# Performance work log

Measured on AMD Instinct MI355X. Metric: run time of the kernel, lower is better.

The kernel has to match this reference:

```python
import math
import jax, jax.numpy as jnp
import numpy as np

# dims: layers, batch, seq, hidden, heads, ffn-mult
L, B, S, D, H, FFN = 2, 4, 2048, 256, 8, 4
HD = D // H          # head dim (= head v dim, double_v_dim=False)
EPS = 1e-5
SCALE_BASE = 512


def _ln(x, w, b):
    mu = x.mean(-1, keepdims=True)
    var = x.var(-1, keepdims=True)
    return (x - mu) * jax.lax.rsqrt(var + EPS) * w + b


def _xpos_tables():
    half = HD // 2
    sv = (np.arange(0, HD, 2) + 0.4 * HD) / (1.4 * HD)            # [half]
    pos = np.arange(S, dtype=np.float64)
    scale = sv[None, :] ** (pos[:, None] / SCALE_BASE)            # [S, half]
    inv_freq = 1.0 / (10000.0 ** (np.arange(half) / half))
    ang = pos[:, None] * inv_freq[None, :]                        # [S, half]
    return (jnp.asarray(np.sin(ang), jnp.float32),
            jnp.asarray(np.cos(ang), jnp.float32),
            jnp.asarray(scale, jnp.float32))

SIN, COS, XSCALE = _xpos_tables()


def _xpos(x, downscale=False):
    # x: [B, H, S, HD]
    sc = 1.0 / XSCALE if downscale else XSCALE
    sin2 = jnp.repeat(SIN * sc, 2, axis=-1)                       # [S, HD]
    cos2 = jnp.repeat(COS * sc, 2, axis=-1)
    x1, x2 = x[..., 0::2], x[..., 1::2]
    xr = jnp.stack((-x2, x1), axis=-1).reshape(x.shape)           # rotate_every_two
    return x * cos2 + xr * sin2


def _decay_mask():
    g = 1.0 - jnp.exp(jnp.linspace(math.log(1 / 32), math.log(1 / 512), H))
    n = jnp.arange(S)[:, None]
    m = jnp.arange(S)[None, :]
    keep = n >= m
    expo = jnp.where(keep, n - m, 0).astype(jnp.float32)
    return jnp.where(keep, g[:, None, None] ** expo[None], 0.0)   # [H, S, S]

DMASK = _decay_mask()


def setup_inputs() -> dict:
    key = jax.random.key(0)
    ks = jax.random.split(key, 16)
    sc = 1.0 / D
    f32 = jnp.float32
    return {
        "X":     jax.random.normal(ks[0], (B, S, D), f32),
        "Wq":    jax.random.normal(ks[1], (L, D, D), f32) * sc,
        "Wk":    jax.random.normal(ks[2], (L, D, D), f32) * sc,
        "Wv":    jax.random.normal(ks[3], (L, D, D), f32) * sc,
        "Wg":    jax.random.normal(ks[4], (L, D, D), f32) * sc,
        "Wo":    jax.random.normal(ks[5], (L, D, D), f32) * sc,
        "gn_w":  jnp.ones((L, D), f32) + 0.02 * jax.random.normal(ks[6], (L, D), f32),
        "gn_b":  0.02 * jax.random.normal(ks[7], (L, D), f32),
        "ln1_w": jnp.ones((L, D), f32),
        "ln1_b": jnp.zeros((L, D), f32),
        "ln2_w": jnp.ones((L, D), f32),
        "ln2_b": jnp.zeros((L, D), f32),
        "w1":    jax.random.normal(ks[8], (L, D, FFN * D), f32) * 0.02,
        "b1":    0.02 * jax.random.normal(ks[9], (L, FFN * D), f32),
        "w2":    jax.random.normal(ks[10], (L, FFN * D, D), f32) * 0.02,
        "b2":    0.02 * jax.random.normal(ks[11], (L, D), f32),
        "lnf_w": jnp.ones((D,), f32),
        "lnf_b": jnp.zeros((D,), f32),
    }


def reference(X, Wq, Wk, Wv, Wg, Wo, gn_w, gn_b, ln1_w, ln1_b,
              ln2_w, ln2_b, w1, b1, w2, b2, lnf_w, lnf_b):
    x = X
    for i in range(L):
        xn = _ln(x, ln1_w[i], ln1_b[i])                           # [B,S,D]
        q = (xn @ Wq[i]).reshape(B, S, H, HD).transpose(0, 2, 1, 3)
        k = (xn @ Wk[i]).reshape(B, S, H, HD).transpose(0, 2, 1, 3)
        v = (xn @ Wv[i]).reshape(B, S, H, HD).transpose(0, 2, 1, 3)
        q = _xpos(q)
        k = _xpos(k, downscale=True)
        att = jnp.einsum('bhnd,bhmd->bhnm', q, k) * DMASK          # [B,H,S,S]
        y = jnp.einsum('bhnm,bhmd->bhnd', att, v)                  # [B,H,S,HD]
        # GroupNorm(heads, v_dim): per-(b, position, head) normalization
        mu = y.mean(-1, keepdims=True)
        var = y.var(-1, keepdims=True)
        y = (y - mu) * jax.lax.rsqrt(var + EPS)
        y = y.transpose(0, 2, 1, 3).reshape(B, S, D)               # concat heads
        y = y * gn_w[i] + gn_b[i]
        g = xn @ Wg[i]
        ret = (g * jax.nn.sigmoid(g) * y) @ Wo[i]                  # swish gate + out proj
        yres = ret + x
        yn = _ln(yres, ln2_w[i], ln2_b[i])
        f = jax.nn.gelu(yn @ w1[i] + b1[i], approximate=False) @ w2[i] + b2[i]
        x = _ln(f + yres, lnf_w, lnf_b)
    return x
```

## Files before the change

kernel.cpp:

```cpp
#include <hip/hip_runtime.h>
#include <hip/hip_bf16.h>

typedef __hip_bfloat16 bf16;
typedef unsigned short ushort_t;
typedef __attribute__((ext_vector_type(8))) short short8v;
typedef __attribute__((ext_vector_type(4))) float f32x4;
typedef __attribute__((ext_vector_type(4))) unsigned int uint4v;

#define LYR 2
#define BB 4
#define SS 2048
#define DD 256
#define HH 8
#define HDD 32
#define FFD 1024
#define MM (BB*SS)

__device__ __forceinline__ unsigned int cvtpk(float lo, float hi) {
  unsigned int r;
  asm("v_cvt_pk_bf16_f32 %0, %1, %2" : "=v"(r) : "v"(lo), "v"(hi));
  return r;
}
__device__ __forceinline__ ushort_t f2b1(float x) { return (ushort_t)cvtpk(x, x); }

__device__ __forceinline__ void gload_lds16(const void* g, void* l) {
  __builtin_amdgcn_global_load_lds((const __attribute__((address_space(1))) void*)g,
                                   (__attribute__((address_space(3))) void*)l, 16, 0, 0);
}

__device__ __forceinline__ float l2g_of(int h) {
  return log2f(1.0f - expf(-3.4657359028f - 0.3960841187f * (float)h));
}

struct WDesc { const float* src; bf16* dst; int K; int N; };
struct WDescA { WDesc d[14]; float* tsn; float* tcs; float* tsc; };
__global__ __launch_bounds__(256) void wconv_k(WDescA da) {
  if (blockIdx.z == 14) {
    int i = (blockIdx.y * 32 + blockIdx.x) * 256 + threadIdx.y * 32 + threadIdx.x;
    if (i >= SS * 16) return;
    int s = i >> 4, j = i & 15;
    float sv = (2.0f * (float)j + 0.4f * (float)HDD) / (1.4f * (float)HDD);
    da.tsc[i] = powf(sv, (float)s * (1.0f / 512.0f));
    float inv_freq = powf(10000.0f, -(float)j * (1.0f / 16.0f));
    float ang = (float)s * inv_freq;
    da.tsn[i] = sinf(ang);
    da.tcs[i] = cosf(ang);
    return;
  }
  WDesc dd = da.d[blockIdx.z];
  int n0 = blockIdx.x * 32, k0 = blockIdx.y * 32;
  if (n0 >= dd.N || k0 >= dd.K) return;
  __shared__ float t[32][33];
  int tx = threadIdx.x, ty = threadIdx.y;
  #pragma unroll
  for (int i = 0; i < 32; i += 8) t[ty + i][tx] = dd.src[(size_t)(k0 + ty + i) * dd.N + n0 + tx];
  __syncthreads();
  #pragma unroll
  for (int i = 0; i < 32; i += 8) dd.dst[(size_t)(n0 + ty + i) * dd.K + k0 + tx] = __float2bfloat16(t[tx][ty + i]);
}

template<typename OT>
__global__ __launch_bounds__(256) void ln_k(const float* __restrict__ in, const float* __restrict__ w,
    const float* __restrict__ b, OT* __restrict__ out)
{
  int row = blockIdx.x, t = threadIdx.x;
  float v = in[(size_t)row * DD + t];
  __shared__ float red[4];
  float s = v;
  #pragma unroll
  for (int m = 32; m >= 1; m >>= 1) s += __shfl_xor(s, m);
  if ((t & 63) == 0) red[t >> 6] = s;
  __syncthreads();
  float mu = (red[0] + red[1] + red[2] + red[3]) * (1.0f / 256.0f);
  float d = v - mu;
  float s2 = d * d;
  #pragma unroll
  for (int m = 32; m >= 1; m >>= 1) s2 += __shfl_xor(s2, m);
  __syncthreads();
  if ((t & 63) == 0) red[t >> 6] = s2;
  __syncthreads();
  float var = (red[0] + red[1] + red[2] + red[3]) * (1.0f / 256.0f);
  float o = d * rsqrtf(var + 1e-5f) * w[t] + b[t];
  if constexpr (sizeof(OT) == 2) out[(size_t)row * DD + t] = __float2bfloat16(o);
  else                           out[(size_t)row * DD + t] = o;
}

#define STAGEG(buf, k0s) { \
    _Pragma("unroll") \
    for (int i = 0; i < BM / 32; ++i) { \
      int slot = i * 256 + tid; int row = slot >> 3, blk = slot & 7; \
      gload_lds16(Au + (size_t)(bm + row) * K + (k0s) + ((blk ^ (row & 7))) * 8, &Al[buf][slot * 8]); \
    } \
    _Pragma("unroll") \
    for (int i = 0; i < BN / 32; ++i) { \
      int slot = i * 256 + tid; int row = slot >> 3, blk = slot & 7; \
      gload_lds16(Bu + (size_t)(bn + row) * K + (k0s) + ((blk ^ (row & 7))) * 8, &Bl[buf][slot * 8]); \
    } }

enum { E_QKVG = 0 };

template<int BM, int BN, int K, int EPI>
__global__ __launch_bounds__(256) void mgemm_k(const bf16* __restrict__ Ag, const bf16* __restrict__ Wt,
    void* o0, void* o1, void* o2, void* o3,
    const float* __restrict__ tsn, const float* __restrict__ tcs, const float* __restrict__ tsc)
{
  constexpr int MT = BM / 32, NT = BN / 32;
  constexpr int WMH = BM / 2, WNH = BN / 2;
  __shared__ __align__(16) ushort_t Al[2][BM * 64];
  __shared__ __align__(16) ushort_t Bl[2][BN * 64];
  const int bm = blockIdx.x * BM;
  const int bn = blockIdx.y * BN;
  const int tid = threadIdx.x;
  const int lane = tid & 63, w = tid >> 6;
  const int lg = lane >> 4, ln = lane & 15;
  const int wr = w >> 1, wc = w & 1;
  const ushort_t* Au = (const ushort_t*)Ag;
  const ushort_t* Bu = (const ushort_t*)Wt;
  f32x4 acc[MT][NT] = {};

  STAGEG(0, 0)
  asm volatile("s_waitcnt vmcnt(0)" ::: "memory");
  __builtin_amdgcn_s_barrier();

  int cur = 0;
  for (int k0 = 0; k0 < K; k0 += 64) {
    if (k0 + 64 < K) STAGEG(cur ^ 1, k0 + 64)
    #pragma unroll
    for (int kh = 0; kh < 2; ++kh) {
      short8v af[MT], bfr[NT];
      #pragma unroll
      for (int mt = 0; mt < MT; ++mt) {
        int row = wr * WMH + mt * 16 + ln;
        af[mt] = *(const short8v*)&Al[cur][row * 64 + (((kh * 4 + lg) ^ (row & 7))) * 8];
      }
      #pragma unroll
      for (int nt = 0; nt < NT; ++nt) {
        int row = wc * WNH + nt * 16 + ln;
        bfr[nt] = *(const short8v*)&Bl[cur][row * 64 + (((kh * 4 + lg) ^ (row & 7))) * 8];
      }
      #pragma unroll
      for (int mt = 0; mt < MT; ++mt)
        #pragma unroll
        for (int nt = 0; nt < NT; ++nt)
          acc[mt][nt] = __builtin_amdgcn_mfma_f32_16x16x32_bf16(af[mt], bfr[nt], acc[mt][nt], 0, 0, 0);
    }
    asm volatile("s_waitcnt vmcnt(0)" ::: "memory");
    __builtin_amdgcn_s_barrier();
    cur ^= 1;
  }

  #pragma unroll
  for (int mt = 0; mt < MT; ++mt)
    #pragma unroll
    for (int nt = 0; nt < NT; ++nt) {
      const int colbase = bn + wc * WNH + nt * 16;
      const int sec = colbase >> 8;
      const int c = (colbase & 255) + ln;
      const int grow0 = bm + wr * WMH + mt * 16 + lg * 4;
      if (sec <= 1) {
        const int jj = (c & 31) >> 1;
        const float l2g = l2g_of(c >> 5);
        #pragma unroll
        for (int r = 0; r < 4; ++r) {
          const int grow = grow0 + r;
          const int s = grow & (SS - 1);
          float v = acc[mt][nt][r];
          float pv = __shfl_xor(v, 1);
          float scv = tsc[s * 16 + jj];
          if (sec == 1) scv = 1.0f / scv;
          float ce = tcs[s * 16 + jj] * scv, se = tsn[s * 16 + jj] * scv;
          float o = (ln & 1) ? (v * ce + pv * se) : (v * ce - pv * se);
          if (sec == 0) o *= exp2f(l2g * (float)s);
          bf16* dst = (sec == 0) ? (bf16*)o0 : (bf16*)o1;
          dst[(size_t)grow * DD + c] = __float2bfloat16(o);
        }
      } else if (sec == 2) {
        const int b = grow0 >> 11, s0 = grow0 & (SS - 1);
        const int h = c >> 5, d = c & 31;
        const float nl2g = -l2g_of(h);
        float v0 = acc[mt][nt][0] * exp2f(nl2g * (float)(s0 + 0));
        float v1 = acc[mt][nt][1] * exp2f(nl2g * (float)(s0 + 1));
        float v2 = acc[mt][nt][2] * exp2f(nl2g * (float)(s0 + 2));
        float v3 = acc[mt][nt][3] * exp2f(nl2g * (float)(s0 + 3));
        uint2 pk;
        pk.x = cvtpk(v0, v1);
        pk.y = cvtpk(v2, v3);
        *(uint2*)((ushort_t*)o2 + ((size_t)(b * 8 + h) * 32 + d) * SS + s0) = pk;
      } else {
        #pragma unroll
        for (int r = 0; r < 4; ++r)
          ((float*)o3)[(size_t)(grow0 + r) * DD + c] = acc[mt][nt][r];
      }
    }
}

template<bool LAST>
__global__ __launch_bounds__(256, 3) void ffn_mega(
    const bf16* __restrict__ ubg, const bf16* __restrict__ wotg,
    const bf16* __restrict__ w1tg, const bf16* __restrict__ w2tg,
    const float* __restrict__ b1v, const float* __restrict__ b2v,
    const float* __restrict__ resin,
    float* __restrict__ yres, bf16* __restrict__ xn, float* __restrict__ dout,
    const float* __restrict__ l2w, const float* __restrict__ l2b,
    const float* __restrict__ lfw, const float* __restrict__ lfb,
    const float* __restrict__ l1w, const float* __restrict__ l1b)
{
  __shared__ __align__(16) ushort_t Bs[4][4096];
  __shared__ __align__(16) ushort_t AX[4096];
  __shared__ __align__(16) ushort_t Us[4096];

  const int bm = blockIdx.x * 16;
  const int tid = threadIdx.x;
  const int lane = tid & 63, w = tid >> 6;
  const int lg = lane >> 4, ln = lane & 15;
  const int row0 = lg * 4;
  const ushort_t* ubu  = (const ushort_t*)ubg;
  const ushort_t* wotu = (const ushort_t*)wotg;
  const ushort_t* w1tu = (const ushort_t*)w1tg;
  const ushort_t* w2tu = (const ushort_t*)w2tg;
  float* red = (float*)Us;

  float resv[4][4];
  #pragma unroll
  for (int nt = 0; nt < 4; ++nt) {
    const int gcol = w * 64 + nt * 16 + ln;
    #pragma unroll
    for (int r = 0; r < 4; ++r)
      resv[nt][r] = resin[(size_t)(bm + row0 + r) * DD + gcol];
  }

  #define STAGEBW(base, stride, nbase, koff) { \
    _Pragma("unroll") \
    for (int i = 0; i < 8; ++i) { \
      int slot = i * 64 + lane; int r = slot >> 3, blk = slot & 7; \
      gload_lds16((base) + (size_t)((nbase) + w * 64 + r) * (stride) + (koff) + ((blk ^ (r & 7))) * 8, &Bs[w][slot * 8]); \
    } }
  #define STAGEA(buf, koff) { \
    if (tid < 128) { int rr = tid >> 3, blk = tid & 7; \
      gload_lds16(ubu + (size_t)(bm + rr) * DD + (koff) + ((blk ^ (rr & 7))) * 8, &AX[(buf) * 1024 + tid * 8]); } }
  #define WAVEWAIT asm volatile("s_waitcnt vmcnt(0)" ::: "memory");

  STAGEA(0, 0)
  STAGEBW(wotu, 256, 0, 0)
  WAVEWAIT
  __builtin_amdgcn_s_barrier();
  int cur = 0;
  f32x4 accw[4] = {};
  #pragma unroll
  for (int s = 0; s < 4; ++s) {
    if (s < 3) STAGEA(cur ^ 1, (s + 1) * 64)
    #pragma unroll
    for (int kh = 0; kh < 2; ++kh) {
      short8v af = *(const short8v*)&AX[cur * 1024 + ln * 64 + (((kh * 4 + lg) ^ (ln & 7))) * 8];
      #pragma unroll
      for (int nt = 0; nt < 4; ++nt) {
        int r = nt * 16 + ln;
        short8v bf_ = *(const short8v*)&Bs[w][r * 64 + (((kh * 4 + lg) ^ (r & 7))) * 8];
        accw[nt] = __builtin_amdgcn_mfma_f32_16x16x32_bf16(af, bf_, accw[nt], 0, 0, 0);
      }
    }
    if (s < 3) STAGEBW(wotu, 256, 0, (s + 1) * 64)
    WAVEWAIT
    __builtin_amdgcn_s_barrier();
    cur ^= 1;
  }

  float v[4][4];
  #pragma unroll
  for (int nt = 0; nt < 4; ++nt)
    #pragma unroll
    for (int r = 0; r < 4; ++r) v[nt][r] = accw[nt][r] + resv[nt][r];
  float mu[4], rsg[4];
  {
    #pragma unroll
    for (int r = 0; r < 4; ++r) {
      float s1 = 0.f, s2 = 0.f;
      #pragma unroll
      for (int nt = 0; nt < 4; ++nt) { s1 += v[nt][r]; s2 += v[nt][r] * v[nt][r]; }
      #pragma unroll
      for (int m = 8; m >= 1; m >>= 1) { s1 += __shfl_xor(s1, m); s2 += __shfl_xor(s2, m); }
      if (ln == 0) { red[(w * 16 + row0 + r) * 2] = s1; red[(w * 16 + row0 + r) * 2 + 1] = s2; }
    }
    __syncthreads();
    #pragma unroll
    for (int r = 0; r < 4; ++r) {
      float S = 0.f, S2 = 0.f;
      #pragma unroll
      for (int ww = 0; ww < 4; ++ww) { S += red[(ww * 16 + row0 + r) * 2]; S2 += red[(ww * 16 + row0 + r) * 2 + 1]; }
      float m_ = S * (1.0f / 256.0f);
      mu[r] = m_; rsg[r] = rsqrtf(S2 * (1.0f / 256.0f) - m_ * m_ + 1e-5f);
    }
  }
  #pragma unroll
  for (int nt = 0; nt < 4; ++nt) {
    const int gcol = w * 64 + nt * 16 + ln;
    const float lwv = l2w[gcol], lbv = l2b[gcol];
    const int off = nt * 16 + ln, blk = off >> 3, sub = off & 7;
    #pragma unroll
    for (int r = 0; r < 4; ++r) {
      const int row = row0 + r;
      float xv = (v[nt][r] - mu[r]) * rsg[r] * lwv + lbv;
      AX[row * 256 + w * 64 + ((blk ^ (row & 7)) << 3) + sub] = f2b1(xv);
    }
  }
  __syncthreads();

  f32x4 acc2[4] = {};
  #pragma unroll
  for (int c = 0; c < 4; ++c) {
    f32x4 acc1[4] = {};
    #pragma unroll
    for (int s = 0; s < 4; ++s) {
      STAGEBW(w1tu, 256, c * 256, s * 64)
      WAVEWAIT
      #pragma unroll
      for (int kh = 0; kh < 2; ++kh) {
        short8v af = *(const short8v*)&AX[ln * 256 + s * 64 + (((kh * 4 + lg) ^ (ln & 7))) * 8];
        #pragma unroll
        for (int nt = 0; nt < 4; ++nt) {
          int r = nt * 16 + ln;
          short8v bf_ = *(const short8v*)&Bs[w][r * 64 + (((kh * 4 + lg) ^ (r & 7))) * 8];
          acc1[nt] = __builtin_amdgcn_mfma_f32_16x16x32_bf16(af, bf_, acc1[nt], 0, 0, 0);
        }
      }
    }
    __syncthreads();
    #pragma unroll
    for (int nt = 0; nt < 4; ++nt) {
      const int gcol1 = c * 256 + w * 64 + nt * 16 + ln;
      const float bb = b1v[gcol1];
      const int off = nt * 16 + ln, blk = off >> 3, sub = off & 7;
      #pragma unroll
      for (int r = 0; r < 4; ++r) {
        const int row = row0 + r;
        float t = acc1[nt][r] + bb;
        t = 0.5f * t * (1.0f + erff(t * 0.70710678118654752f));
        Us[row * 256 + w * 64 + ((blk ^ (row & 7)) << 3) + sub] = f2b1(t);
      }
    }
    __syncthreads();
    #pragma unroll
    for (int s = 0; s < 4; ++s) {
      STAGEBW(w2tu, 1024, 0, c * 256 + s * 64)
      WAVEWAIT
      #pragma unroll
      for (int kh = 0; kh < 2; ++kh) {
        short8v af = *(const short8v*)&Us[ln * 256 + s * 64 + (((kh * 4 + lg) ^ (ln & 7))) * 8];
        #pragma unroll
        for (int nt = 0; nt < 4; ++nt) {
          int r = nt * 16 + ln;
          short8v bf_ = *(const short8v*)&Bs[w][r * 64 + (((kh * 4 + lg) ^ (r & 7))) * 8];
          acc2[nt] = __builtin_amdgcn_mfma_f32_16x16x32_bf16(af, bf_, acc2[nt], 0, 0, 0);
        }
      }
    }
  }
  __syncthreads();

  float f[4][4];
  #pragma unroll
  for (int nt = 0; nt < 4; ++nt) {
    const int gcol = w * 64 + nt * 16 + ln;
    const float bb = b2v[gcol];
    #pragma unroll
    for (int r = 0; r < 4; ++r) f[nt][r] = acc2[nt][r] + bb + v[nt][r];
  }
  {
    #pragma unroll
    for (int r = 0; r < 4; ++r) {
      float s1 = 0.f, s2 = 0.f;
      #pragma unroll
      for (int nt = 0; nt < 4; ++nt) { s1 += f[nt][r]; s2 += f[nt][r] * f[nt][r]; }
      #pragma unroll
      for (int m = 8; m >= 1; m >>= 1) { s1 += __shfl_xor(s1, m); s2 += __shfl_xor(s2, m); }
      if (ln == 0) { red[(w * 16 + row0 + r) * 2] = s1; red[(w * 16 + row0 + r) * 2 + 1] = s2; }
    }
    __syncthreads();
    #pragma unroll
    for (int r = 0; r < 4; ++r) {
      float S = 0.f, S2 = 0.f;
      #pragma unroll
      for (int ww = 0; ww < 4; ++ww) { S += red[(ww * 16 + row0 + r) * 2]; S2 += red[(ww * 16 + row0 + r) * 2 + 1]; }
      float m_ = S * (1.0f / 256.0f);
      mu[r] = m_; rsg[r] = rsqrtf(S2 * (1.0f / 256.0f) - m_ * m_ + 1e-5f);
    }
  }
  float u[4][4];
  #pragma unroll
  for (int nt = 0; nt < 4; ++nt) {
    const int gcol = w * 64 + nt * 16 + ln;
    const float lwv = lfw[gcol], lbv = lfb[gcol];
    #pragma unroll
    for (int r = 0; r < 4; ++r)
      u[nt][r] = (f[nt][r] - mu[r]) * rsg[r] * lwv + lbv;
  }
  if constexpr (LAST) {
    #pragma unroll
    for (int nt = 0; nt < 4; ++nt) {
      const int gcol = w * 64 + nt * 16 + ln;
      #pragma unroll
      for (int r = 0; r < 4; ++r)
        dout[(size_t)(bm + row0 + r) * DD + gcol] = u[nt][r];
    }
  } else {
    __syncthreads();
    #pragma unroll
    for (int r = 0; r < 4; ++r) {
      float s1 = 0.f, s2 = 0.f;
      #pragma unroll
      for (int nt = 0; nt < 4; ++nt) { s1 += u[nt][r]; s2 += u[nt][r] * u[nt][r]; }
      #pragma unroll
      for (int m = 8; m >= 1; m >>= 1) { s1 += __shfl_xor(s1, m); s2 += __shfl_xor(s2, m); }
      if (ln == 0) { red[(w * 16 + row0 + r) * 2] = s1; red[(w * 16 + row0 + r) * 2 + 1] = s2; }
    }
    __syncthreads();
    float mu2[4], rs2[4];
    #pragma unroll
    for (int r = 0; r < 4; ++r) {
      float S = 0.f, S2 = 0.f;
      #pragma unroll
      for (int ww = 0; ww < 4; ++ww) { S += red[(ww * 16 + row0 + r) * 2]; S2 += red[(ww * 16 + row0 + r) * 2 + 1]; }
      float m_ = S * (1.0f / 256.0f);
      mu2[r] = m_; rs2[r] = rsqrtf(S2 * (1.0f / 256.0f) - m_ * m_ + 1e-5f);
    }
    #pragma unroll
    for (int nt = 0; nt < 4; ++nt) {
      const int gcol = w * 64 + nt * 16 + ln;
      const float lwv = l1w[gcol], lbv = l1b[gcol];
      #pragma unroll
      for (int r = 0; r < 4; ++r) {
        const size_t idx = (size_t)(bm + row0 + r) * DD + gcol;
        yres[idx] = u[nt][r];
        xn[idx] = __float2bfloat16((u[nt][r] - mu2[r]) * rs2[r] * lwv + lbv);
      }
    }
  }
  #undef STAGEBW
  #undef STAGEA
  #undef WAVEWAIT
}

__global__ __launch_bounds__(256) void attn_k(const bf16* __restrict__ qg, const bf16* __restrict__ kg,
    const bf16* __restrict__ vtg, const float* __restrict__ gbuf,
    const float* __restrict__ gnw, const float* __restrict__ gnb, bf16* __restrict__ ub)
{
  __shared__ __align__(16) ushort_t Kl[2][64 * 32];
  __shared__ __align__(16) ushort_t Vl[2][32 * 64];
  __shared__ __align__(16) unsigned int Pl[4][512];

  const int bh = blockIdx.x;
  const int b = bh >> 3, h = bh & (HH - 1);
  const int n0 = ((int)gridDim.y - 1 - (int)blockIdx.y) * 64;
  const int tid = threadIdx.x;
  const int w = tid >> 6, lane = tid & 63;
  const int lg = lane >> 4, ln = lane & 15;

  const size_t base = (size_t)b * SS * DD + h * HDD;
  const ushort_t* qp = (const ushort_t*)qg + base;
  const ushort_t* kp = (const ushort_t*)kg + base;
  const ushort_t* vtp = (const ushort_t*)vtg + (size_t)(b * 8 + h) * 32 * SS;

  const int n = n0 + w * 16 + ln;
  const short8v qf = *(const short8v*)(qp + (size_t)n * DD + lg * 8);

  const float l2g = l2g_of(h);
  f32x4 acc0 = {0,0,0,0}, acc1 = {0,0,0,0};

  const int Wwin = (int)(20.0f / (-l2g)) + 1;
  int m_lo = 0;
  if (n0 > Wwin) m_lo = ((n0 - Wwin) >> 6) << 6;

  const int Krow = tid >> 2, Kc8 = tid & 3;
  const int Vrow = tid >> 3, Vc8 = tid & 7;

  #define STAGE(buf, m0s) { \
    gload_lds16(kp + (size_t)((m0s) + Krow) * DD + ((Kc8 ^ (Krow & 3)) * 8), &Kl[buf][tid * 8]); \
    gload_lds16(vtp + (size_t)Vrow * SS + (m0s) + ((Vc8 ^ (Vrow & 7)) * 8), &Vl[buf][tid * 8]); }

  STAGE(0, m_lo)
  asm volatile("s_waitcnt vmcnt(0)" ::: "memory");
  __builtin_amdgcn_s_barrier();

  int cur = 0;
  for (int m0 = m_lo; m0 <= n0; m0 += 64) {
    if (m0 < n0) STAGE(cur ^ 1, m0 + 64)
    const bool diag = (m0 == n0);
    __builtin_amdgcn_s_setprio(1);
    #pragma unroll
    for (int mt = 0; mt < 4; ++mt) {
      const int krow = mt * 16 + ln;
      short8v kf = *(const short8v*)&Kl[cur][krow * 32 + ((lg ^ (krow & 3)) << 3)];
      f32x4 z = {0,0,0,0};
      f32x4 pa = __builtin_amdgcn_mfma_f32_16x16x32_bf16(kf, qf, z, 0, 0, 0);
      float v0 = pa[0], v1 = pa[1], v2 = pa[2], v3 = pa[3];
      if (diag) {
        const int m = n0 + mt * 16 + lg * 4;
        v0 = (n < m)     ? 0.f : v0;
        v1 = (n < m + 1) ? 0.f : v1;
        v2 = (n < m + 2) ? 0.f : v2;
        v3 = (n < m + 3) ? 0.f : v3;
      }
      uint2 pk;
      pk.x = cvtpk(v0, v1);
      pk.y = cvtpk(v2, v3);
      const int blk = (mt * 2 + (lg >> 1)) ^ (ln & 7);
      *(uint2*)&Pl[w][ln * 32 + blk * 4 + (lg & 1) * 2] = pk;
    }
    #pragma unroll
    for (int hh = 0; hh < 2; ++hh) {
      const int pblk = (hh * 4 + lg) ^ (ln & 7);
      uint4v pw = *(const uint4v*)&Pl[w][ln * 32 + pblk * 4];
      short8v pf = __builtin_bit_cast(short8v, pw);
      #pragma unroll
      for (int dt = 0; dt < 2; ++dt) {
        const int d = dt * 16 + ln;
        short8v vf = *(const short8v*)&Vl[cur][d * 64 + (((hh * 4 + lg) ^ (d & 7)) << 3)];
        if (dt == 0) acc0 = __builtin_amdgcn_mfma_f32_16x16x32_bf16(vf, pf, acc0, 0, 0, 0);
        else         acc1 = __builtin_amdgcn_mfma_f32_16x16x32_bf16(vf, pf, acc1, 0, 0, 0);
      }
    }
    __builtin_amdgcn_s_setprio(0);
    asm volatile("s_waitcnt vmcnt(0)" ::: "memory");
    __builtin_amdgcn_s_barrier();
    cur ^= 1;
  }
  #undef STAGE

  float gwv[8], gbv[8];
  #pragma unroll
  for (int dt = 0; dt < 2; ++dt) {
    f32x4 a = *(const f32x4*)&gnw[h * 32 + dt * 16 + lg * 4];
    f32x4 c = *(const f32x4*)&gnb[h * 32 + dt * 16 + lg * 4];
    #pragma unroll
    for (int r = 0; r < 4; ++r) { gwv[dt * 4 + r] = a[r]; gbv[dt * 4 + r] = c[r]; }
  }
  float s = 0.f;
  #pragma unroll
  for (int r = 0; r < 4; ++r) s += acc0[r] + acc1[r];
  s += __shfl_xor(s, 16); s += __shfl_xor(s, 32);
  const float mu = s * (1.0f / 32.0f);
  float s2 = 0.f;
  #pragma unroll
  for (int r = 0; r < 4; ++r) { float d0 = acc0[r] - mu, d1 = acc1[r] - mu; s2 += d0 * d0 + d1 * d1; }
  s2 += __shfl_xor(s2, 16); s2 += __shfl_xor(s2, 32);
  const float rs = rsqrtf(s2 * (1.0f / 32.0f) + 1e-5f);
  const size_t rowoff = ((size_t)b * SS + n) * DD + h * 32;
  #pragma unroll
  for (int dt = 0; dt < 2; ++dt) {
    f32x4 yv = dt ? acc1 : acc0;
    f32x4 gv = *(const f32x4*)&gbuf[rowoff + dt * 16 + lg * 4];
    float o0, o1, o2, o3;
    {
      float yn0 = (yv[0] - mu) * rs * gwv[dt * 4 + 0] + gbv[dt * 4 + 0];
      float yn1 = (yv[1] - mu) * rs * gwv[dt * 4 + 1] + gbv[dt * 4 + 1];
      float yn2 = (yv[2] - mu) * rs * gwv[dt * 4 + 2] + gbv[dt * 4 + 2];
      float yn3 = (yv[3] - mu) * rs * gwv[dt * 4 + 3] + gbv[dt * 4 + 3];
      o0 = gv[0] / (1.0f + expf(-gv[0])) * yn0;
      o1 = gv[1] / (1.0f + expf(-gv[1])) * yn1;
      o2 = gv[2] / (1.0f + expf(-gv[2])) * yn2;
      o3 = gv[3] / (1.0f + expf(-gv[3])) * yn3;
    }
    uint2 pk;
    pk.x = cvtpk(o0, o1);
    pk.y = cvtpk(o2, o3);
    *(uint2*)((ushort_t*)ub + rowoff + dt * 16 + lg * 4) = pk;
  }
}

extern "C" void kernel_launch(void* const* d_in, const int* in_sizes, int n_in,
                              void* d_out, int out_size, void* d_ws, size_t ws_size,
                              hipStream_t stream)
{
  const float* X    = (const float*)d_in[0];
  const float* Wq   = (const float*)d_in[1];
  const float* Wk   = (const float*)d_in[2];
  const float* Wv   = (const float*)d_in[3];
  const float* Wg   = (const float*)d_in[4];
  const float* Wo   = (const float*)d_in[5];
  const float* gnw  = (const float*)d_in[6];
  const float* gnb  = (const float*)d_in[7];
  const float* ln1w = (const float*)d_in[8];
  const float* ln1b = (const float*)d_in[9];
  const float* ln2w = (const float*)d_in[10];
  const float* ln2b = (const float*)d_in[11];
  const float* w1   = (const float*)d_in[12];
  const float* b1   = (const float*)d_in[13];
  const float* w2   = (const float*)d_in[14];
  const float* b2   = (const float*)d_in[15];
  const float* lnfw = (const float*)d_in[16];
  const float* lnfb = (const float*)d_in[17];

  char* p = (char*)d_ws;
  const size_t AF  = (size_t)MM * DD * sizeof(float);
  const size_t ABF = (size_t)MM * DD * sizeof(bf16);
  bf16*  xn   = (bf16*)p;  p += ABF;
  bf16*  qb   = (bf16*)p;  p += ABF;
  bf16*  kb   = (bf16*)p;  p += ABF;
  bf16*  vT   = (bf16*)p;  p += ABF;
  bf16*  ub   = (bf16*)p;  p += ABF;
  float* gbuf = (float*)p; p += AF;
  float* yres = (float*)p; p += AF;
  bf16*  wqkvgt = (bf16*)p; p += (size_t)2 * 1024 * 256 * sizeof(bf16);
  bf16*  wot    = (bf16*)p; p += (size_t)2 * 256 * 256 * sizeof(bf16);
  bf16*  w1t    = (bf16*)p; p += (size_t)2 * 1024 * 256 * sizeof(bf16);
  bf16*  w2t    = (bf16*)p; p += (size_t)2 * 256 * 1024 * sizeof(bf16);
  float* tsn  = (float*)p; p += SS * 16 * sizeof(float);
  float* tcs  = (float*)p; p += SS * 16 * sizeof(float);
  float* tsc  = (float*)p; p += SS * 16 * sizeof(float);

  {
    WDescA da;
    for (int l = 0; l < 2; ++l) {
      da.d[l * 7 + 0] = { Wq + (size_t)l * 65536, wqkvgt + (size_t)l * 262144 + 0 * 65536, 256, 256 };
      da.d[l * 7 + 1] = { Wk + (size_t)l * 65536, wqkvgt + (size_t)l * 262144 + 1 * 65536, 256, 256 };
      da.d[l * 7 + 2] = { Wv + (size_t)l * 65536, wqkvgt + (size_t)l * 262144 + 2 * 65536, 256, 256 };
      da.d[l * 7 + 3] = { Wg + (size_t)l * 65536, wqkvgt + (size_t)l * 262144 + 3 * 65536, 256, 256 };
      da.d[l * 7 + 4] = { Wo + (size_t)l * 65536, wot + (size_t)l * 65536, 256, 256 };
      da.d[l * 7 + 5] = { w1 + (size_t)l * 262144, w1t + (size_t)l * 262144, 256, 1024 };
      da.d[l * 7 + 6] = { w2 + (size_t)l * 262144, w2t + (size_t)l * 262144, 1024, 256 };
    }
    da.tsn = tsn; da.tcs = tcs; da.tsc = tsc;
    wconv_k<<<dim3(32, 32, 15), dim3(32, 8), 0, stream>>>(da);
  }

  ln_k<bf16><<<dim3(MM), 256, 0, stream>>>(X, ln1w, ln1b, xn);

  for (int l = 0; l < LYR; ++l) {
    mgemm_k<64, 128, DD, E_QKVG><<<dim3(MM / 64, 1024 / 128), 256, 0, stream>>>(
        xn, wqkvgt + (size_t)l * 262144, qb, kb, vT, gbuf, tsn, tcs, tsc);
    attn_k<<<dim3(BB * HH, SS / 64), 256, 0, stream>>>(qb, kb, vT, gbuf, gnw + l * DD, gnb + l * DD, ub);
    if (l == LYR - 1) {
      ffn_mega<true><<<dim3(MM / 16), 256, 0, stream>>>(
          ub, wot + (size_t)l * 65536, w1t + (size_t)l * 262144, w2t + (size_t)l * 262144,
          b1 + l * FFD, b2 + l * DD, (l == 0) ? X : yres,
          nullptr, nullptr, (float*)d_out,
          ln2w + l * DD, ln2b + l * DD, lnfw, lnfb, nullptr, nullptr);
    } else {
      ffn_mega<false><<<dim3(MM / 16), 256, 0, stream>>>(
          ub, wot + (size_t)l * 65536, w1t + (size_t)l * 262144, w2t + (size_t)l * 262144,
          b1 + l * FFD, b2 + l * DD, (l == 0) ? X : yres,
          yres, xn, nullptr,
          ln2w + l * DD, ln2b + l * DD, lnfw, lnfb, ln1w + (l + 1) * DD, ln1b + (l + 1) * DD);
    }
  }
}
```

Baseline: 192.0 us.

## Double-buffer per-wave weight staging in ffn_mega to overlap loads with MFMA

Weight tiles for the Wo, W1 and W2 GEMMs now go into two per-wave LDS buffers, and the next tile (including the first tile of the next GEMM) is prefetched before computing on the current one. A partial vmcnt wait replaces the full drain, so global-to-LDS loads overlap MFMA work. The A operand of the Wo GEMM is loaded directly into registers and the b1 biases are hoisted into registers. The cost is double the per-wave B staging LDS and more registers, so launch bounds drop from 3 to 2 blocks per CU, lowering occupancy.

```diff
diff --git a/kernel.cpp b/kernel.cpp
--- a/kernel.cpp
+++ b/kernel.cpp
@@ -195,7 +195,7 @@
 }
 
 template<bool LAST>
-__global__ __launch_bounds__(256, 3) void ffn_mega(
+__global__ __launch_bounds__(256, 2) void ffn_mega(
     const bf16* __restrict__ ubg, const bf16* __restrict__ wotg,
     const bf16* __restrict__ w1tg, const bf16* __restrict__ w2tg,
     const float* __restrict__ b1v, const float* __restrict__ b2v,
@@ -205,8 +205,8 @@
     const float* __restrict__ lfw, const float* __restrict__ lfb,
     const float* __restrict__ l1w, const float* __restrict__ l1b)
 {
-  __shared__ __align__(16) ushort_t Bs[4][4096];
-  __shared__ __align__(16) ushort_t AX[4096];
+  __shared__ __align__(16) ushort_t Bs[4][2][4096];
+  __shared__ __align__(16) ushort_t Xs[4096];
   __shared__ __align__(16) ushort_t Us[4096];
 
   const int bm = blockIdx.x * 16;
@@ -228,41 +228,54 @@
     for (int r = 0; r < 4; ++r)
       resv[nt][r] = resin[(size_t)(bm + row0 + r) * DD + gcol];
   }
-
-  #define STAGEBW(base, stride, nbase, koff) { \
+  float b1r[4][4];
+  #pragma unroll
+  for (int c = 0; c < 4; ++c)
+    #pragma unroll
+    for (int nt = 0; nt < 4; ++nt)
+      b1r[c][nt] = b1v[c * 256 + w * 64 + nt * 16 + ln];
+  short8v aw[4][2];
+  #pragma unroll
+  for (int s = 0; s < 4; ++s)
+    #pragma unroll
+    for (int kh = 0; kh < 2; ++kh)
+      aw[s][kh] = *(const short8v*)(ubu + (size_t)(bm + ln) * DD + s * 64 + kh * 32 + lg * 8);
+
+  #define STAGEBW(base, stride, nbase, koff, par) { \
     _Pragma("unroll") \
     for (int i = 0; i < 8; ++i) { \
       int slot = i * 64 + lane; int r = slot >> 3, blk = slot & 7; \
-      gload_lds16((base) + (size_t)((nbase) + w * 64 + r) * (stride) + (koff) + ((blk ^ (r & 7))) * 8, &Bs[w][slot * 8]); \
+      gload_lds16((base) + (size_t)((nbase) + w * 64 + r) * (stride) + (koff) + ((blk ^ (r & 7))) * 8, &Bs[w][par][slot * 8]); \
     } }
-  #define STAGEA(buf, koff) { \
-    if (tid < 128) { int rr = tid >> 3, blk = tid & 7; \
-      gload_lds16(ubu + (size_t)(bm + rr) * DD + (koff) + ((blk ^ (rr & 7))) * 8, &AX[(buf) * 1024 + tid * 8]); } }
-  #define WAVEWAIT asm volatile("s_waitcnt vmcnt(0)" ::: "memory");
-
-  STAGEA(0, 0)
-  STAGEBW(wotu, 256, 0, 0)
-  WAVEWAIT
-  __builtin_amdgcn_s_barrier();
-  int cur = 0;
+  #define VMW8 asm volatile("s_waitcnt vmcnt(8)" ::: "memory");
+  #define VMW0 asm volatile("s_waitcnt vmcnt(0)" ::: "memory");
+  #define FSTEP(Aarr, s, par, accv) { \
+    _Pragma("unroll") \
+    for (int kh = 0; kh < 2; ++kh) { \
+      short8v af = *(const short8v*)&Aarr[ln * 256 + (s) * 64 + (((kh * 4 + lg) ^ (ln & 7))) * 8]; \
+      _Pragma("unroll") \
+      for (int nt = 0; nt < 4; ++nt) { \
+        int r = nt * 16 + ln; \
+        short8v bf_ = *(const short8v*)&Bs[w][par][r * 64 + (((kh * 4 + lg) ^ (r & 7))) * 8]; \
+        accv[nt] = __builtin_amdgcn_mfma_f32_16x16x32_bf16(af, bf_, accv[nt], 0, 0, 0); \
+      } } }
+
+  STAGEBW(wotu, 256, 0, 0, 0)
+
   f32x4 accw[4] = {};
   #pragma unroll
   for (int s = 0; s < 4; ++s) {
-    if (s < 3) STAGEA(cur ^ 1, (s + 1) * 64)
-    #pragma unroll
-    for (int kh = 0; kh < 2; ++kh) {
-      short8v af = *(const short8v*)&AX[cur * 1024 + ln * 64 + (((kh * 4 + lg) ^ (ln & 7))) * 8];
+    if (s < 3) STAGEBW(wotu, 256, 0, (s + 1) * 64, (s + 1) & 1)
+    else       STAGEBW(w1tu, 256, 0, 0, 0)
+    VMW8
+    #pragma unroll
+    for (int kh = 0; kh < 2; ++kh)
       #pragma unroll
       for (int nt = 0; nt < 4; ++nt) {
         int r = nt * 16 + ln;
-        short8v bf_ = *(const short8v*)&Bs[w][r * 64 + (((kh * 4 + lg) ^ (r & 7))) * 8];
-        accw[nt] = __builtin_amdgcn_mfma_f32_16x16x32_bf16(af, bf_, accw[nt], 0, 0, 0);
-      }
-    }
-    if (s < 3) STAGEBW(wotu, 256, 0, (s + 1) * 64)
-    WAVEWAIT
-    __builtin_amdgcn_s_barrier();
-    cur ^= 1;
+        short8v bf_ = *(const short8v*)&Bs[w][s & 1][r * 64 + (((kh * 4 + lg) ^ (r & 7))) * 8];
+        accw[nt] = __builtin_amdgcn_mfma_f32_16x16x32_bf16(aw[s][kh], bf_, accw[nt], 0, 0, 0);
+      }
   }
 
   float v[4][4];
@@ -300,7 +313,7 @@
     for (int r = 0; r < 4; ++r) {
       const int row = row0 + r;
       float xv = (v[nt][r] - mu[r]) * rsg[r] * lwv + lbv;
-      AX[row * 256 + w * 64 + ((blk ^ (row & 7)) << 3) + sub] = f2b1(xv);
+      Xs[row * 256 + w * 64 + ((blk ^ (row & 7)) << 3) + sub] = f2b1(xv);
     }
   }
   __syncthreads();
@@ -311,24 +324,15 @@
     f32x4 acc1[4] = {};
     #pragma unroll
     for (int s = 0; s < 4; ++s) {
-      STAGEBW(w1tu, 256, c * 256, s * 64)
-      WAVEWAIT
-      #pragma unroll
-      for (int kh = 0; kh < 2; ++kh) {
-        short8v af = *(const short8v*)&AX[ln * 256 + s * 64 + (((kh * 4 + lg) ^ (ln & 7))) * 8];
-        #pragma unroll
-        for (int nt = 0; nt < 4; ++nt) {
-          int r = nt * 16 + ln;
-          short8v bf_ = *(const short8v*)&Bs[w][r * 64 + (((kh * 4 + lg) ^ (r & 7))) * 8];
-          acc1[nt] = __builtin_amdgcn_mfma_f32_16x16x32_bf16(af, bf_, acc1[nt], 0, 0, 0);
-        }
-      }
+      if (s < 3) STAGEBW(w1tu, 256, c * 256, (s + 1) * 64, (s + 1) & 1)
+      else       STAGEBW(w2tu, 1024, 0, c * 256, 0)
+      VMW8
+      FSTEP(Xs, s, s & 1, acc1)
     }
     __syncthreads();
     #pragma unroll
     for (int nt = 0; nt < 4; ++nt) {
-      const int gcol1 = c * 256 + w * 64 + nt * 16 + ln;
-      const float bb = b1v[gcol1];
+      const float bb = b1r[c][nt];
       const int off = nt * 16 + ln, blk = off >> 3, sub = off & 7;
       #pragma unroll
       for (int r = 0; r < 4; ++r) {
@@ -341,18 +345,10 @@
     __syncthreads();
     #pragma unroll
     for (int s = 0; s < 4; ++s) {
-      STAGEBW(w2tu, 1024, 0, c * 256 + s * 64)
-      WAVEWAIT
-      #pragma unroll
-      for (int kh = 0; kh < 2; ++kh) {
-        short8v af = *(const short8v*)&Us[ln * 256 + s * 64 + (((kh * 4 + lg) ^ (ln & 7))) * 8];
-        #pragma unroll
-        for (int nt = 0; nt < 4; ++nt) {
-          int r = nt * 16 + ln;
-          short8v bf_ = *(const short8v*)&Bs[w][r * 64 + (((kh * 4 + lg) ^ (r & 7))) * 8];
-          acc2[nt] = __builtin_amdgcn_mfma_f32_16x16x32_bf16(af, bf_, acc2[nt], 0, 0, 0);
-        }
-      }
+      if (s < 3)      STAGEBW(w2tu, 1024, 0, c * 256 + (s + 1) * 64, (s + 1) & 1)
+      else if (c < 3) STAGEBW(w1tu, 256, (c + 1) * 256, 0, 0)
+      if (c == 3 && s == 3) { VMW0 } else { VMW8 }
+      FSTEP(Us, s, s & 1, acc2)
     }
   }
   __syncthreads();
@@ -436,8 +432,9 @@
     }
   }
   #undef STAGEBW
-  #undef STAGEA
-  #undef WAVEWAIT
+  #undef VMW8
+  #undef VMW0
+  #undef FSTEP
 }
 
 __global__ __launch_bounds__(256) void attn_k(const bf16* __restrict__ qg, const bf16* __restrict__ kg,
```

Result: faster. 185.1 us (-3.6%).
